# Performance work log

Hardware: AMD Instinct MI355X
Metric: run time of the kernel (lower is better)

## Reference

```python
import jax, jax.numpy as jnp
import numpy as np

L = 4   # num_encoders
H = 8   # num_heads
D = 49  # dim_in == dim_proj == dim_out == num_patches
B = 2048
NCLS = 10
HID = 25
SCALE = np.sqrt(D).astype(np.float32) + 1e-6  # sqrt(49)+eps as in torch code


def setup_inputs() -> dict:
    key = jax.random.key(0)
    ks = jax.random.split(key, 16)
    s = 0.05
    inp = {
        'embedding': jax.random.normal(ks[0], (B, D, D), dtype=jnp.float32),
        'target_labels': jax.random.randint(ks[1], (B,), 0, NCLS, dtype=jnp.int32),
        # per-layer, per-head attention weights, stored [in, out] (torch Linear applies x @ W.T + b)
        'Wq': jax.random.normal(ks[2], (L, H, D, D), dtype=jnp.float32) * s,
        'bq': jnp.zeros((L, H, D), dtype=jnp.float32),
        'Wk': jax.random.normal(ks[3], (L, H, D, D), dtype=jnp.float32) * s,
        'bk': jnp.zeros((L, H, D), dtype=jnp.float32),
        'Wv': jax.random.normal(ks[4], (L, H, D, D), dtype=jnp.float32) * s,
        'bv': jnp.zeros((L, H, D), dtype=jnp.float32),
        'Wh': jax.random.normal(ks[5], (L, H, D, D), dtype=jnp.float32) * s,
        'bh': jnp.zeros((L, H, D), dtype=jnp.float32),
        # W_out_proj is Linear(392,49) used WITHOUT bias (matmul with weight.t());
        # reshape [392,49] -> [H,49,49] so concat-over-heads @ Wout.T == einsum over h.
        'Wout': jax.random.normal(ks[6], (L, H, D, D), dtype=jnp.float32) * s,
        # mlp_between_blocks: two Linears, NO activation (faithful to source)
        'W1': jax.random.normal(ks[7], (L, D, D), dtype=jnp.float32) * s,
        'b1': jnp.zeros((L, D), dtype=jnp.float32),
        'W2': jax.random.normal(ks[8], (L, D, D), dtype=jnp.float32) * s,
        'b2': jnp.zeros((L, D), dtype=jnp.float32),
        # cls head MLP 49 -> 25 -> 10, no activation
        'Wc1': jax.random.normal(ks[9], (D, HID), dtype=jnp.float32) * s,
        'bc1': jnp.zeros((HID,), dtype=jnp.float32),
        'Wc2': jax.random.normal(ks[10], (HID, NCLS), dtype=jnp.float32) * s,
        'bc2': jnp.zeros((NCLS,), dtype=jnp.float32),
    }
    return inp


def reference(embedding, target_labels, Wq, bq, Wk, bk, Wv, bv, Wh, bh, Wout,
              W1, b1, W2, b2, Wc1, bc1, Wc2, bc2):
    x = embedding  # [B, N=49, D=49]
    for l in range(L):
        # batched over heads: [B,N,D] x [H,D,E] -> [B,H,N,E]
        Q = jnp.einsum('bnd,hde->bhne', x, Wq[l]) + bq[l][None, :, None, :]
        K = jnp.einsum('bnd,hde->bhne', x, Wk[l]) + bk[l][None, :, None, :]
        V = jnp.einsum('bnd,hde->bhne', x, Wv[l]) + bv[l][None, :, None, :]
        scores = jnp.einsum('bhne,bhme->bhnm', Q, K) / SCALE
        scores = jnp.clip(scores, -30.0, 30.0)
        attn = jax.nn.softmax(scores, axis=-1)
        ctx = jnp.einsum('bhnm,bhme->bhne', attn, V)
        head_out = jnp.einsum('bhne,heo->bhno', ctx, Wh[l]) + bh[l][None, :, None, :]
        # concat over heads then Linear(392,49) without bias == sum over h of per-head proj
        x = jnp.einsum('bhno,hod->bnd', head_out, Wout[l])
        # mlp_between_blocks (no activation)
        x = (x @ W1[l] + b1[l]) @ W2[l] + b2[l]
    pooled = x.mean(axis=1)                       # [B, 49]
    logits = (pooled @ Wc1 + bc1) @ Wc2 + bc2     # [B, 10]
    logp = jax.nn.log_softmax(logits, axis=-1)
    loss = -jnp.take_along_axis(logp, target_labels[:, None].astype(jnp.int32), axis=1).mean()
    pred = jnp.argmax(logits, axis=1)
    accuracy = (pred == target_labels).astype(jnp.float32).sum() / logits.shape[0]
    return loss, accuracy
```

## Files before the change

### kernel.cpp

```cpp
#include <hip/hip_runtime.h>
#include <math.h>

namespace {

constexpr int D    = 49;
constexpr int H    = 8;
constexpr int L    = 4;
constexpr int HID  = 25;
constexpr int NCLS = 10;
constexpr int XS   = 68;
constexpr int WSM  = 4096;
constexpr float SCLF  = 1.44269504088896f / (7.0f + 1e-6f);
constexpr float CLIP2 = 30.0f * 1.44269504088896f;

typedef __attribute__((ext_vector_type(4))) short short4v;
typedef __attribute__((ext_vector_type(8))) short short8v;
typedef __attribute__((ext_vector_type(4))) float float4v;
typedef __attribute__((ext_vector_type(8))) __bf16 bf16x8;

__device__ __forceinline__ float4v mfma32(short8v a, short8v b, float4v c) {
  return __builtin_amdgcn_mfma_f32_16x16x32_bf16(a, b, c, 0, 0, 0);
}

__device__ __forceinline__ unsigned short f2bf(float x) {
  unsigned u = __float_as_uint(x);
  return (unsigned short)((u + 0x7FFFu + ((u >> 16) & 1u)) >> 16);
}

__device__ __forceinline__ short8v cvt8(float4v lo, float4v hi) {
  bf16x8 b = {(__bf16)lo[0], (__bf16)lo[1], (__bf16)lo[2], (__bf16)lo[3],
              (__bf16)hi[0], (__bf16)hi[1], (__bf16)hi[2], (__bf16)hi[3]};
  return __builtin_bit_cast(short8v, b);
}

__device__ __forceinline__ float exp2_hw(float x) {
  float r;
  asm("v_exp_f32 %0, %1" : "=v"(r) : "v"(x));
  return r;
}

__device__ __forceinline__ float4v splat4(float x) {
  float4v v; v[0] = x; v[1] = x; v[2] = x; v[3] = x; return v;
}

__device__ __forceinline__ short8v wsld8(const unsigned short* __restrict__ w,
                                         int t, int nt, int lane) {
  return *reinterpret_cast<const short8v*>(w + ((t * 4 + nt) * 64 + lane) * 8);
}

__device__ __forceinline__ void mmT8(const unsigned short* __restrict__ w,
                                     const short8v (&src)[2][4],
                                     int lane, float4v (&acc)[4][4]) {
  #pragma unroll
  for (int mt = 0; mt < 4; ++mt)
    #pragma unroll
    for (int nt = 0; nt < 4; ++nt) acc[mt][nt] = splat4(0.0f);
  #pragma unroll
  for (int t = 0; t < 2; ++t) {
    short8v a[4];
    #pragma unroll
    for (int mt = 0; mt < 4; ++mt) a[mt] = wsld8(w, t, mt, lane);
    #pragma unroll
    for (int nt = 0; nt < 4; ++nt)
      #pragma unroll
      for (int mt = 0; mt < 4; ++mt)
        acc[mt][nt] = mfma32(a[mt], src[t][nt], acc[mt][nt]);
  }
}

__device__ __forceinline__ void pack_from_lds(const float* __restrict__ M,
                                              const float* __restrict__ biasRow,
                                              float diag,
                                              unsigned short* __restrict__ dst,
                                              int tid) {
  const int lane = tid & 63;
  const int gg = (lane >> 4) & 3, cc = lane & 15;
  #pragma unroll
  for (int i = 0; i < 2; ++i) {
    const int p = ((tid >> 6) << 1) | i;
    const int tt = p >> 2, nt = p & 3;
    short8v v;
    #pragma unroll
    for (int j = 0; j < 8; ++j) {
      const int k = 32 * tt + ((j < 4) ? (4 * gg + j) : (16 + 4 * gg + j - 4));
      const int n = 16 * nt + cc;
      float f = 0.0f;
      if (k < D && n < D)        f = M[k * D + n];
      else if (k == D) {
        if (n < D)               f = biasRow[n];
        else if (n == D)         f = diag;
      }
      v[j] = (short)f2bf(f);
    }
    *reinterpret_cast<short8v*>(dst + ((tt * 4 + nt) * 64 + lane) * 8) = v;
  }
}

__device__ __forceinline__ void lds_mm(const float* __restrict__ A49,
                                       const float* __restrict__ B49,
                                       float* __restrict__ OUT, int tid) {
  for (int i = tid; i < D * D; i += 256) {
    const int r = i / D, c = i - r * D;
    float s = 0.0f;
    #pragma unroll
    for (int k = 0; k < D; ++k) s = fmaf(A49[r * D + k], B49[k * D + c], s);
    OUT[i] = s;
  }
}

__global__ void __launch_bounds__(256)
prep_all(const float* __restrict__ Wq, const float* __restrict__ bq,
         const float* __restrict__ Wk, const float* __restrict__ bk,
         const float* __restrict__ Wv, const float* __restrict__ bv,
         const float* __restrict__ Wh, const float* __restrict__ bh,
         const float* __restrict__ Wout,
         const float* __restrict__ W1, const float* __restrict__ b1,
         const float* __restrict__ W2, const float* __restrict__ b2,
         unsigned short* __restrict__ ws) {
  __shared__ float MA[D * D], MB[D * D], MT[D * D];
  __shared__ float BR[64], CH[64], BH[8 * 64];
  const int m = blockIdx.x;
  const int tid = threadIdx.x;
  unsigned short* dst = ws + (size_t)m * WSM;

  if (m < 64) {
    const int hh = (m < 32) ? m : (m - 32);
    const float scl = (m < 32) ? 1.0f : SCLF;
    const float* src = ((m < 32) ? Wq : Wk) + (size_t)hh * D * D;
    const float* bsr = ((m < 32) ? bq : bk) + hh * D;
    for (int i = tid; i < D * D; i += 256) MT[i] = src[i] * scl;
    if (tid < D) BR[tid] = bsr[tid] * scl;
    __syncthreads();
    pack_from_lds(MT, BR, 0.0f, dst, tid);
    return;
  }

  if (m < 96) {
    const int lh = m - 64;
    const float* wh = Wh + (size_t)lh * D * D;
    const float* wo = Wout + (size_t)lh * D * D;
    const float* wv = Wv + (size_t)lh * D * D;
    for (int i = tid; i < D * D; i += 256) { MA[i] = wh[i]; MB[i] = wo[i]; }
    __syncthreads();
    lds_mm(MA, MB, MT, tid);
    __syncthreads();
    for (int i = tid; i < D * D; i += 256) MA[i] = wv[i];
    if (tid < D) {
      float s = 0.0f;
      #pragma unroll
      for (int k = 0; k < D; ++k) s = fmaf(bv[lh * D + k], MT[k * D + tid], s);
      BR[tid] = s;
    }
    __syncthreads();
    lds_mm(MA, MT, MB, tid);
    __syncthreads();
    pack_from_lds(MB, BR, 0.125f, dst, tid);
    return;
  }

  const int l = m - 96;
  for (int i = tid; i < D * D; i += 256) {
    MA[i] = W1[(size_t)l * D * D + i];
    MB[i] = W2[(size_t)l * D * D + i];
  }
  for (int i = tid; i < H * D; i += 256)
    BH[(i / D) * 64 + (i % D)] = bh[(l * H + (i / D)) * D + (i % D)];
  __syncthreads();
  if (tid < D) {
    float s = 0.0f;
    #pragma unroll
    for (int h = 0; h < H; ++h) {
      const size_t base = (size_t)(l * H + h) * D * D;
      #pragma unroll
      for (int k = 0; k < D; ++k)
        s = fmaf(BH[h * 64 + k], Wout[base + k * D + tid], s);
    }
    CH[tid] = s;
  }
  __syncthreads();
  lds_mm(MA, MB, MT, tid);
  __syncthreads();
  if (tid < D) {
    float s = b2[l * D + tid];
    #pragma unroll
    for (int k = 0; k < D; ++k) {
      s = fmaf(b1[l * D + k], MB[k * D + tid], s);
      s = fmaf(CH[k], MT[k * D + tid], s);
    }
    BR[tid] = s;
  }
  __syncthreads();
  pack_from_lds(MT, BR, 1.0f, dst, tid);
}

__global__ void __launch_bounds__(64, 2)
encoder_kernel(const float* __restrict__ emb, const int* __restrict__ labels,
               const unsigned short* __restrict__ ws,
               const float* __restrict__ Wc1, const float* __restrict__ bc1,
               const float* __restrict__ Wc2, const float* __restrict__ bc2,
               float* __restrict__ ws_loss, float* __restrict__ ws_corr) {
  __shared__ unsigned short X[64 * XS];
  __shared__ float CLS[128];

  const int b = blockIdx.x;
  const int lane = threadIdx.x;
  const int g = lane >> 4, c = lane & 15;

  for (int idx = lane; idx < 64 * 64; idx += 64) {
    const int r = idx >> 6, cc = idx & 63;
    float v = 0.0f;
    if (cc == D) v = 1.0f;
    else if (r < D && cc < D) v = emb[(size_t)b * (D * D) + r * D + cc];
    X[r * XS + cc] = f2bf(v);
  }
  __syncthreads();

  short8v xf8[2][4];
  #pragma unroll
  for (int t = 0; t < 2; ++t)
    #pragma unroll
    for (int nt = 0; nt < 4; ++nt) {
      const int base = (16 * nt + c) * XS + 32 * t + 4 * g;
      short4v lo = *reinterpret_cast<const short4v*>(&X[base]);
      short4v hi = *reinterpret_cast<const short4v*>(&X[base + 16]);
      xf8[t][nt] = __builtin_shufflevector(lo, hi, 0, 1, 2, 3, 4, 5, 6, 7);
    }

  float4v xacc[4][4];

  #pragma unroll 1
  for (int l = 0; l < L; ++l) {
    float4v od[4][4];
    #pragma unroll
    for (int mt = 0; mt < 4; ++mt)
      #pragma unroll
      for (int nt = 0; nt < 4; ++nt) od[mt][nt] = splat4(0.0f);

    #pragma unroll 2
    for (int h = 0; h < H; ++h) {
      const int lh = l * H + h;
      const unsigned short* wq = ws + (size_t)(0  + lh) * WSM;
      const unsigned short* wk = ws + (size_t)(32 + lh) * WSM;
      const unsigned short* wf = ws + (size_t)(64 + lh) * WSM;

      short8v kf8[2][4], qf8[2][4];
      {
        float4v ka[4][4];
        mmT8(wk, xf8, lane, ka);
        #pragma unroll
        for (int t = 0; t < 2; ++t)
          #pragma unroll
          for (int nt = 0; nt < 4; ++nt)
            kf8[t][nt] = cvt8(ka[2 * t][nt], ka[2 * t + 1][nt]);
      }
      {
        float4v qa[4][4];
        mmT8(wq, xf8, lane, qa);
        #pragma unroll
        for (int t = 0; t < 2; ++t)
          #pragma unroll
          for (int nt = 0; nt < 4; ++nt)
            qf8[t][nt] = cvt8(qa[2 * t][nt], qa[2 * t + 1][nt]);
      }

      short8v uf8[2][4];
      {
        float4v ua[4][4];
        #pragma unroll
        for (int nt = 0; nt < 4; ++nt)
          #pragma unroll
          for (int mt = 0; mt < 4; ++mt) ua[mt][nt] = splat4(0.0f);
        #pragma unroll
        for (int t = 0; t < 2; ++t) {
          short8v wff[4];
          #pragma unroll
          for (int nt = 0; nt < 4; ++nt) wff[nt] = wsld8(wf, t, nt, lane);
          #pragma unroll
          for (int nt = 0; nt < 4; ++nt)
            #pragma unroll
            for (int mt = 0; mt < 4; ++mt)
              ua[mt][nt] = mfma32(xf8[t][mt], wff[nt], ua[mt][nt]);
        }
        #pragma unroll
        for (int t = 0; t < 2; ++t)
          #pragma unroll
          for (int nt = 0; nt < 4; ++nt)
            uf8[t][nt] = cvt8(ua[2 * t][nt], ua[2 * t + 1][nt]);
      }

      #pragma unroll
      for (int nt = 0; nt < 4; ++nt) {
        float4v sc[4];
        #pragma unroll
        for (int mt = 0; mt < 4; ++mt) sc[mt] = splat4(0.0f);
        #pragma unroll
        for (int t = 0; t < 2; ++t)
          #pragma unroll
          for (int mt = 0; mt < 4; ++mt)
            sc[mt] = mfma32(kf8[t][mt], qf8[t][nt], sc[mt]);

        #pragma unroll
        for (int mt = 0; mt < 4; ++mt)
          #pragma unroll
          for (int r = 0; r < 4; ++r) {
            if (mt == 3 && r > 0) { sc[mt][r] = 0.0f; continue; }
            const float sv = fminf(fmaxf(sc[mt][r], -CLIP2), CLIP2);
            float p = exp2_hw(sv);
            if (mt == 3) p = (g == 0) ? p : 0.0f;
            sc[mt][r] = p;
          }
        const short8v pf0 = cvt8(sc[0], sc[1]);
        const short8v pf1 = cvt8(sc[2], sc[3]);

        float4v cc[4];
        #pragma unroll
        for (int mt = 0; mt < 4; ++mt) cc[mt] = splat4(0.0f);
        #pragma unroll
        for (int mt = 0; mt < 4; ++mt) {
          cc[mt] = mfma32(uf8[0][mt], pf0, cc[mt]);
          cc[mt] = mfma32(uf8[1][mt], pf1, cc[mt]);
        }
        const float inv = 0.125f / __shfl(cc[3][1], c);
        const float4v iv = splat4(inv);
        #pragma unroll
        for (int mt = 0; mt < 4; ++mt)
          od[mt][nt] += cc[mt] * iv;
      }
    }

    short8v of8[2][4];
    #pragma unroll
    for (int t = 0; t < 2; ++t)
      #pragma unroll
      for (int nt = 0; nt < 4; ++nt)
        of8[t][nt] = cvt8(od[2 * t][nt], od[2 * t + 1][nt]);
    mmT8(ws + (size_t)(96 + l) * WSM, of8, lane, xacc);

    if (l < L - 1) {
      #pragma unroll
      for (int t = 0; t < 2; ++t)
        #pragma unroll
        for (int nt = 0; nt < 4; ++nt)
          xf8[t][nt] = cvt8(xacc[2 * t][nt], xacc[2 * t + 1][nt]);
    }
  }

  #pragma unroll
  for (int mt = 0; mt < 4; ++mt) {
    #pragma unroll
    for (int r = 0; r < 4; ++r) {
      float sv = xacc[mt][0][r] + xacc[mt][1][r] + xacc[mt][2][r];
      if (c == 0) sv += xacc[mt][3][r];
      sv += __shfl_xor(sv, 1);
      sv += __shfl_xor(sv, 2);
      sv += __shfl_xor(sv, 4);
      sv += __shfl_xor(sv, 8);
      if (c == 0) CLS[16 * mt + 4 * g + r] = sv * (1.0f / 49.0f);
    }
  }
  __syncthreads();

  if (lane < HID) {
    float acc = bc1[lane];
    #pragma unroll
    for (int d = 0; d < D; ++d) acc = fmaf(CLS[d], Wc1[d * HID + lane], acc);
    CLS[64 + lane] = acc;
  }
  __syncthreads();
  if (lane < NCLS) {
    float acc = bc2[lane];
    #pragma unroll
    for (int j = 0; j < HID; ++j) acc = fmaf(CLS[64 + j], Wc2[j * NCLS + lane], acc);
    CLS[96 + lane] = acc;
  }
  __syncthreads();
  if (lane == 0) {
    float mx = CLS[96];
    int am = 0;
    #pragma unroll 1
    for (int cc2 = 1; cc2 < NCLS; ++cc2) {
      const float v = CLS[96 + cc2];
      if (v > mx) { mx = v; am = cc2; }
    }
    float se = 0.0f;
    #pragma unroll 1
    for (int cc2 = 0; cc2 < NCLS; ++cc2) se += expf(CLS[96 + cc2] - mx);
    const float lse = mx + logf(se);
    const int lbl = labels[b];
    ws_loss[b] = lse - CLS[96 + lbl];
    ws_corr[b] = (am == lbl) ? 1.0f : 0.0f;
  }
}

__global__ void __launch_bounds__(256)
reduce_kernel(const float* __restrict__ wsl, const float* __restrict__ wsc,
              float* __restrict__ out, int n) {
  __shared__ float sl[256];
  __shared__ float sc[256];
  const int t = threadIdx.x;
  float a = 0.0f, cc = 0.0f;
  for (int idx = t; idx < n; idx += 256) { a += wsl[idx]; cc += wsc[idx]; }
  sl[t] = a; sc[t] = cc;
  __syncthreads();
  for (int s = 128; s > 0; s >>= 1) {
    if (t < s) { sl[t] += sl[t + s]; sc[t] += sc[t + s]; }
    __syncthreads();
  }
  if (t == 0) {
    out[0] = sl[0] / (float)n;
    out[1] = sc[0] / (float)n;
  }
}

}

extern "C" void kernel_launch(void* const* d_in, const int* in_sizes, int n_in,
                              void* d_out, int out_size, void* d_ws, size_t ws_size,
                              hipStream_t stream) {
  const float* emb    = (const float*)d_in[0];
  const int*   labels = (const int*)d_in[1];
  const float* Wq   = (const float*)d_in[2];
  const float* bq   = (const float*)d_in[3];
  const float* Wk   = (const float*)d_in[4];
  const float* bk   = (const float*)d_in[5];
  const float* Wv   = (const float*)d_in[6];
  const float* bv   = (const float*)d_in[7];
  const float* Wh   = (const float*)d_in[8];
  const float* bh   = (const float*)d_in[9];
  const float* Wout = (const float*)d_in[10];
  const float* W1   = (const float*)d_in[11];
  const float* b1   = (const float*)d_in[12];
  const float* W2   = (const float*)d_in[13];
  const float* b2   = (const float*)d_in[14];
  const float* Wc1  = (const float*)d_in[15];
  const float* bc1  = (const float*)d_in[16];
  const float* Wc2  = (const float*)d_in[17];
  const float* bc2  = (const float*)d_in[18];

  const int B = in_sizes[1];
  const size_t fragB = (size_t)100 * WSM * sizeof(unsigned short);
  const size_t need = fragB + (size_t)2 * B * sizeof(float);
  if (ws_size < need) return;

  unsigned short* wsb = (unsigned short*)d_ws;
  float* wsf = (float*)((char*)d_ws + fragB);
  float* out = (float*)d_out;

  prep_all<<<100, 256, 0, stream>>>(Wq, bq, Wk, bk, Wv, bv, Wh, bh, Wout,
                                    W1, b1, W2, b2, wsb);
  encoder_kernel<<<B, 64, 0, stream>>>(emb, labels, wsb, Wc1, bc1, Wc2, bc2,
                                       wsf, wsf + B);
  reduce_kernel<<<1, 256, 0, stream>>>(wsf, wsf + B, out, B);
}
```

Baseline: 170.0 us.

## Fold Wq and Wk into a single bilinear matrix per head

The preprocessing kernel now precomputes M = Wk·Wqᵀ (scaled), plus the bias cross terms, as one augmented 50x50 matrix per head. The encoder computes T = M·x once and forms the scores from T and x directly, instead of projecting both Q and K. This removes one of the three per-head projection matmuls and its bf16 conversion, and cuts the prep grid from 100 to 68 blocks. In exchange the fused product is rounded to bf16, which can change score precision.

Result: faster. 148.7 us (-12.6%).

```diff
diff --git a/kernel.cpp b/kernel.cpp
--- a/kernel.cpp
+++ b/kernel.cpp
@@ -68,11 +68,10 @@
   }
 }
 
-__device__ __forceinline__ void pack_from_lds(const float* __restrict__ M,
-                                              const float* __restrict__ biasRow,
-                                              float diag,
-                                              unsigned short* __restrict__ dst,
-                                              int tid) {
+__device__ __forceinline__ void pack2(const float* __restrict__ M,
+                                      const float* __restrict__ row49,
+                                      const float* __restrict__ col49,
+                                      unsigned short* __restrict__ dst, int tid) {
   const int lane = tid & 63;
   const int gg = (lane >> 4) & 3, cc = lane & 15;
   #pragma unroll
@@ -85,10 +84,11 @@
       const int k = 32 * tt + ((j < 4) ? (4 * gg + j) : (16 + 4 * gg + j - 4));
       const int n = 16 * nt + cc;
       float f = 0.0f;
-      if (k < D && n < D)        f = M[k * D + n];
-      else if (k == D) {
-        if (n < D)               f = biasRow[n];
-        else if (n == D)         f = diag;
+      if (k < D) {
+        if (n < D)       f = M[k * D + n];
+        else if (n == D) f = col49 ? col49[k] : 0.0f;
+      } else if (k == D) {
+        if (n <= D)      f = row49[n];
       }
       v[j] = (short)f2bf(f);
     }
@@ -118,25 +118,49 @@
          const float* __restrict__ W2, const float* __restrict__ b2,
          unsigned short* __restrict__ ws) {
   __shared__ float MA[D * D], MB[D * D], MT[D * D];
-  __shared__ float BR[64], CH[64], BH[8 * 64];
+  __shared__ float BR[64], CL[64], VA[64], VB[64], BH[8 * 64];
   const int m = blockIdx.x;
   const int tid = threadIdx.x;
   unsigned short* dst = ws + (size_t)m * WSM;
 
+  if (m < 32) {
+    const int lh = m;
+    for (int i = tid; i < D * D; i += 256) {
+      MA[i] = Wk[(size_t)lh * D * D + i];
+      MB[i] = Wq[(size_t)lh * D * D + i];
+    }
+    if (tid < D) { VA[tid] = bk[lh * D + tid]; VB[tid] = bq[lh * D + tid]; }
+    __syncthreads();
+    for (int i = tid; i < D * D; i += 256) {
+      const int r = i / D, c = i - r * D;
+      float s = 0.0f;
+      #pragma unroll
+      for (int e = 0; e < D; ++e) s = fmaf(MA[r * D + e], MB[c * D + e], s);
+      MT[i] = s * SCLF;
+    }
+    if (tid < D) {
+      float s = 0.0f, s2 = 0.0f;
+      #pragma unroll
+      for (int e = 0; e < D; ++e) {
+        s  = fmaf(VA[e], MB[tid * D + e], s);
+        s2 = fmaf(MA[tid * D + e], VB[e], s2);
+      }
+      BR[tid] = s * SCLF;
+      CL[tid] = s2 * SCLF;
+    }
+    if (tid == 0) {
+      float s = 0.0f;
+      #pragma unroll
+      for (int e = 0; e < D; ++e) s = fmaf(VA[e], VB[e], s);
+      BR[D] = s * SCLF;
+    }
+    __syncthreads();
+    pack2(MT, BR, CL, dst, tid);
+    return;
+  }
+
   if (m < 64) {
-    const int hh = (m < 32) ? m : (m - 32);
-    const float scl = (m < 32) ? 1.0f : SCLF;
-    const float* src = ((m < 32) ? Wq : Wk) + (size_t)hh * D * D;
-    const float* bsr = ((m < 32) ? bq : bk) + hh * D;
-    for (int i = tid; i < D * D; i += 256) MT[i] = src[i] * scl;
-    if (tid < D) BR[tid] = bsr[tid] * scl;
-    __syncthreads();
-    pack_from_lds(MT, BR, 0.0f, dst, tid);
-    return;
-  }
-
-  if (m < 96) {
-    const int lh = m - 64;
+    const int lh = m - 32;
     const float* wh = Wh + (size_t)lh * D * D;
     const float* wo = Wout + (size_t)lh * D * D;
     const float* wv = Wv + (size_t)lh * D * D;
@@ -151,14 +175,15 @@
       for (int k = 0; k < D; ++k) s = fmaf(bv[lh * D + k], MT[k * D + tid], s);
       BR[tid] = s;
     }
+    if (tid == 0) BR[D] = 0.125f;
     __syncthreads();
     lds_mm(MA, MT, MB, tid);
     __syncthreads();
-    pack_from_lds(MB, BR, 0.125f, dst, tid);
+    pack2(MB, BR, nullptr, dst, tid);
     return;
   }
 
-  const int l = m - 96;
+  const int l = m - 64;
   for (int i = tid; i < D * D; i += 256) {
     MA[i] = W1[(size_t)l * D * D + i];
     MB[i] = W2[(size_t)l * D * D + i];
@@ -175,7 +200,7 @@
       for (int k = 0; k < D; ++k)
         s = fmaf(BH[h * 64 + k], Wout[base + k * D + tid], s);
     }
-    CH[tid] = s;
+    CL[tid] = s;
   }
   __syncthreads();
   lds_mm(MA, MB, MT, tid);
@@ -185,12 +210,13 @@
     #pragma unroll
     for (int k = 0; k < D; ++k) {
       s = fmaf(b1[l * D + k], MB[k * D + tid], s);
-      s = fmaf(CH[k], MT[k * D + tid], s);
+      s = fmaf(CL[k], MT[k * D + tid], s);
     }
     BR[tid] = s;
   }
-  __syncthreads();
-  pack_from_lds(MT, BR, 1.0f, dst, tid);
+  if (tid == 0) BR[D] = 1.0f;
+  __syncthreads();
+  pack2(MT, BR, nullptr, dst, tid);
 }
 
 __global__ void __launch_bounds__(64, 2)
@@ -239,28 +265,18 @@
     #pragma unroll 2
     for (int h = 0; h < H; ++h) {
       const int lh = l * H + h;
-      const unsigned short* wq = ws + (size_t)(0  + lh) * WSM;
-      const unsigned short* wk = ws + (size_t)(32 + lh) * WSM;
-      const unsigned short* wf = ws + (size_t)(64 + lh) * WSM;
-
-      short8v kf8[2][4], qf8[2][4];
+      const unsigned short* wm = ws + (size_t)lh * WSM;
+      const unsigned short* wf = ws + (size_t)(32 + lh) * WSM;
+
+      short8v tf8[2][4];
       {
-        float4v ka[4][4];
-        mmT8(wk, xf8, lane, ka);
+        float4v ta[4][4];
+        mmT8(wm, xf8, lane, ta);
         #pragma unroll
         for (int t = 0; t < 2; ++t)
           #pragma unroll
           for (int nt = 0; nt < 4; ++nt)
-            kf8[t][nt] = cvt8(ka[2 * t][nt], ka[2 * t + 1][nt]);
-      }
-      {
-        float4v qa[4][4];
-        mmT8(wq, xf8, lane, qa);
-        #pragma unroll
-        for (int t = 0; t < 2; ++t)
-          #pragma unroll
-          for (int nt = 0; nt < 4; ++nt)
-            qf8[t][nt] = cvt8(qa[2 * t][nt], qa[2 * t + 1][nt]);
+            tf8[t][nt] = cvt8(ta[2 * t][nt], ta[2 * t + 1][nt]);
       }
 
       short8v uf8[2][4];
@@ -297,7 +313,7 @@
         for (int t = 0; t < 2; ++t)
           #pragma unroll
           for (int mt = 0; mt < 4; ++mt)
-            sc[mt] = mfma32(kf8[t][mt], qf8[t][nt], sc[mt]);
+            sc[mt] = mfma32(tf8[t][mt], xf8[t][nt], sc[mt]);
 
         #pragma unroll
         for (int mt = 0; mt < 4; ++mt)
@@ -334,7 +350,7 @@
       #pragma unroll
       for (int nt = 0; nt < 4; ++nt)
         of8[t][nt] = cvt8(od[2 * t][nt], od[2 * t + 1][nt]);
-    mmT8(ws + (size_t)(96 + l) * WSM, of8, lane, xacc);
+    mmT8(ws + (size_t)(64 + l) * WSM, of8, lane, xacc);
 
     if (l < L - 1) {
       #pragma unroll
@@ -438,7 +454,7 @@
   const float* bc2  = (const float*)d_in[18];
 
   const int B = in_sizes[1];
-  const size_t fragB = (size_t)100 * WSM * sizeof(unsigned short);
+  const size_t fragB = (size_t)68 * WSM * sizeof(unsigned short);
   const size_t need = fragB + (size_t)2 * B * sizeof(float);
   if (ws_size < need) return;
 
@@ -446,8 +462,8 @@
   float* wsf = (float*)((char*)d_ws + fragB);
   float* out = (float*)d_out;
 
-  prep_all<<<100, 256, 0, stream>>>(Wq, bq, Wk, bk, Wv, bv, Wh, bh, Wout,
-                                    W1, b1, W2, b2, wsb);
+  prep_all<<<68, 256, 0, stream>>>(Wq, bq, Wk, bk, Wv, bv, Wh, bh, Wout,
+                                   W1, b1, W2, b2, wsb);
   encoder_kernel<<<B, 64, 0, stream>>>(emb, labels, wsb, Wc1, bc1, Wc2, bc2,
                                        wsf, wsf + B);
   reduce_kernel<<<1, 256, 0, stream>>>(wsf, wsf + B, out, B);
```
